# Kernel optimization log

Hardware: AMD Instinct MI355X
Metric: run time of the kernel (lower is better)

Reference implementation:

```python
import jax, jax.numpy as jnp
import numpy as np

N = 50000
E = 800000
IN_CH = 256
ADIM = 64
EDIM = 16
NUM_CLUSTERS = 8


def setup_inputs() -> dict:
    key = jax.random.key(0)
    ks = jax.random.split(key, 16)
    def lin(k, fan_in, fan_out):
        w = jax.random.normal(k, (fan_in, fan_out), jnp.float32) * (fan_in ** -0.5)
        b = jnp.zeros((fan_out,), jnp.float32)
        return w, b
    W_down, b_down = lin(ks[0], IN_CH, ADIM)
    W_up, b_up = lin(ks[1], ADIM, IN_CH)
    W_time, b_time = lin(ks[2], EDIM, ADIM)
    Wq, bq = lin(ks[3], ADIM, ADIM)
    Wk, bk = lin(ks[4], ADIM, ADIM)
    Wv, bv = lin(ks[5], ADIM, ADIM)
    W_out, b_out = lin(ks[6], ADIM, ADIM)
    cluster_emb = jax.random.normal(ks[7], (NUM_CLUSTERS, ADIM), jnp.float32)
    x = jax.random.normal(ks[8], (N, IN_CH), jnp.float32)
    edge_attr = jax.random.normal(ks[9], (E, EDIM), jnp.float32)
    edge_index = jax.random.randint(ks[10], (2, E), 0, N, jnp.int32)
    return {"x": x, "edge_attr": edge_attr, "edge_index": edge_index,
            "W_down": W_down, "b_down": b_down, "W_up": W_up, "b_up": b_up,
            "W_time": W_time, "b_time": b_time, "Wq": Wq, "bq": bq,
            "Wk": Wk, "bk": bk, "Wv": Wv, "bv": bv,
            "cluster_emb": cluster_emb, "W_out": W_out, "b_out": b_out}


def reference(x, edge_attr, edge_index, W_down, b_down, W_up, b_up,
              W_time, b_time, Wq, bq, Wk, bk, Wv, bv, cluster_emb, W_out, b_out):
    n_nodes = x.shape[0]
    scaling = ADIM ** -0.5

    node_feat = jax.nn.relu(x @ W_down + b_down)              # [N, D]
    time_feat = jax.nn.relu(edge_attr @ W_time + b_time)      # [E, D]

    q = node_feat @ Wq + bq                                   # [N, D]
    k = time_feat @ Wk + bk                                   # [E, D]
    v = time_feat @ Wv + bv                                   # [E, D]

    # cluster assignment: argmax of softmax(sim) == argmax of sim
    sims = (time_feat @ cluster_emb.T) * scaling              # [E, C]
    cluster = jnp.argmax(sims, axis=-1).astype(jnp.int32)     # [E]

    src = edge_index[0]                                       # [E]
    q_i = q[src]                                              # [E, D]
    attn = jnp.sum(q_i * k, axis=-1) * scaling                # [E]

    # per-(cluster, src) segments replicate the per-cluster loop exactly
    seg = cluster * n_nodes + src                             # [E]
    num_seg = NUM_CLUSTERS * n_nodes

    # scatter_softmax within each (cluster, src) group (numerically stable)
    m = jax.ops.segment_max(attn, seg, num_segments=num_seg)
    ex = jnp.exp(attn - m[seg])
    denom = jax.ops.segment_sum(ex, seg, num_segments=num_seg)
    w = ex / denom[seg]                                       # [E]

    wv = v * w[:, None]                                       # [E, D]
    sums = jax.ops.segment_sum(wv, seg, num_segments=num_seg)
    sums = sums.reshape(NUM_CLUSTERS, n_nodes, ADIM)
    counts = jax.ops.segment_sum(jnp.ones((E,), jnp.float32), seg, num_segments=num_seg)
    counts = counts.reshape(NUM_CLUSTERS, n_nodes)
    mean = sums / jnp.maximum(counts, 1.0)[..., None]         # scatter_mean (0 where empty)

    # divide by number of non-empty clusters (len(outputs) in torch loop)
    edges_per_cluster = jax.ops.segment_sum(jnp.ones((E,), jnp.float32), cluster,
                                            num_segments=NUM_CLUSTERS)
    n_nonempty = jnp.sum((edges_per_cluster > 0).astype(jnp.float32))
    combined = jnp.sum(mean, axis=0) / n_nonempty             # [N, D]

    fused = jax.nn.relu(combined @ W_out + b_out)             # [N, D]
    out = x + (fused @ W_up + b_up)                           # [N, in_ch]
    return out
```

## Files before the change

### kernel.cpp

```cpp
#include <hip/hip_runtime.h>

#define NN 50000
#define EE 800000
#define INCH 256
#define D 64
#define ED 16
#define NC 8
#define NB 196
#define NEGINF (-3.0e38f)

__device__ __align__(16) char g_ws[64u << 20];

__device__ __forceinline__ unsigned short f2b(float f){
  unsigned u = __float_as_uint(f);
  return (unsigned short)((u + 0x7fffu + ((u >> 16) & 1u)) >> 16);
}
__device__ __forceinline__ unsigned packbf(float lo, float hi){
  return (unsigned)f2b(lo) | ((unsigned)f2b(hi) << 16);
}
__device__ __forceinline__ float blo(unsigned w){ return __uint_as_float(w << 16); }
__device__ __forceinline__ float bhi(unsigned w){ return __uint_as_float(w & 0xffff0000u); }

__global__ __launch_bounds__(256) void Adapter_30872224923942_kernel(
    unsigned* __restrict__ ws, int nwords)
{
  int stride = gridDim.x * 256;
  for (int i = blockIdx.x * 256 + threadIdx.x; i < nwords; i += stride)
    ws[i] = 0u;
}

__global__ __launch_bounds__(256) void kpre(
    const float* __restrict__ Wq, const float* __restrict__ bq,
    const float* __restrict__ Wk, const float* __restrict__ bk,
    const float* __restrict__ Wv, const float* __restrict__ bv,
    const float* __restrict__ Wo, const float* __restrict__ Wd,
    const float* __restrict__ Wu,
    float* __restrict__ M, float* __restrict__ cvec, float* __restrict__ u,
    float* __restrict__ s0, float* __restrict__ Wvo, float* __restrict__ bvo,
    unsigned* __restrict__ WdP, unsigned* __restrict__ WuP)
{
  int b = blockIdx.x, t = threadIdx.x;
  if (b < 16){
    int i = b*4 + (t >> 6), j = t & 63;
    float acc = 0.0f;
    for (int d = 0; d < D; ++d) acc = fmaf(Wq[i*D+d], Wk[j*D+d], acc);
    M[i*D+j] = acc;
  } else if (b < 32){
    int i = (b-16)*4 + (t >> 6), j = t & 63;
    float acc = 0.0f;
    for (int d = 0; d < D; ++d) acc = fmaf(Wv[i*D+d], Wo[d*D+j], acc);
    Wvo[i*D+j] = acc;
  } else if (b < 36){
    for (int k = 0; k < 8; ++k){
      int idx = (b-32)*2048 + t*8 + k;
      int c2 = idx >> 6, j = idx & 63;
      WdP[idx] = packbf(Wd[(2*c2)*D + j], Wd[(2*c2+1)*D + j]);
    }
  } else if (b < 40){
    for (int k = 0; k < 8; ++k){
      int idx = (b-36)*2048 + t*8 + k;
      int d2 = idx >> 8, c = idx & 255;
      WuP[idx] = packbf(Wu[(2*d2)*INCH + c], Wu[(2*d2+1)*INCH + c]);
    }
  } else {
    if (t < 64){
      float acc = 0.0f;
      for (int d = 0; d < D; ++d) acc = fmaf(Wk[t*D+d], bq[d], acc);
      cvec[t] = acc;
    } else if (t < 128){
      int i = t - 64; float acc = 0.0f;
      for (int d = 0; d < D; ++d) acc = fmaf(Wq[i*D+d], bk[d], acc);
      u[i] = acc;
    } else if (t < 192){
      int j = t - 128; float acc = 0.0f;
      for (int d = 0; d < D; ++d) acc = fmaf(bv[d], Wo[d*D+j], acc);
      bvo[j] = acc;
    } else if (t == 192){
      float acc = 0.0f;
      for (int d = 0; d < D; ++d) acc = fmaf(bq[d], bk[d], acc);
      s0[0] = acc;
    }
  }
}

__global__ __launch_bounds__(256) void p1_hist(
    const int* __restrict__ eidx, int* __restrict__ cnt)
{
  int e = blockIdx.x * 256 + threadIdx.x;
  if (e < EE) atomicAdd(&cnt[eidx[e]], 1);
}

__global__ __launch_bounds__(256) void s1_scan(
    const int* __restrict__ cnt, int* __restrict__ rowptr, int* __restrict__ bsum)
{
  __shared__ int s[256];
  int t = threadIdx.x;
  int i = blockIdx.x * 256 + t;
  int v = (i < NN) ? cnt[i] : 0;
  s[t] = v; __syncthreads();
  #pragma unroll
  for (int off = 1; off < 256; off <<= 1){
    int add = (t >= off) ? s[t - off] : 0;
    __syncthreads();
    s[t] += add;
    __syncthreads();
  }
  if (i < NN) rowptr[i] = s[t] - v;
  if (t == 255) bsum[blockIdx.x] = s[255];
}
__global__ __launch_bounds__(256) void s2_scan(int* __restrict__ bsum)
{
  __shared__ int s[256];
  int t = threadIdx.x;
  int v = (t < NB) ? bsum[t] : 0;
  s[t] = v; __syncthreads();
  #pragma unroll
  for (int off = 1; off < 256; off <<= 1){
    int add = (t >= off) ? s[t - off] : 0;
    __syncthreads();
    s[t] += add;
    __syncthreads();
  }
  if (t < NB) bsum[t] = s[t] - v;
}
__global__ __launch_bounds__(256) void s3_add(
    int* __restrict__ rowptr, const int* __restrict__ bsum)
{
  int i = blockIdx.x * 256 + threadIdx.x;
  if (i < NN) rowptr[i] += bsum[blockIdx.x];
  if (i == 0) rowptr[NN] = EE;
}

__global__ __launch_bounds__(256) void p2_build(
    const int* __restrict__ eidx, const int* __restrict__ rowptr,
    int* __restrict__ fill, int2* __restrict__ pairS)
{
  int e = blockIdx.x * 256 + threadIdx.x;
  if (e >= EE) return;
  int src = eidx[e];
  int r = atomicAdd(&fill[src], 1);
  int2 pr; pr.x = e; pr.y = src;
  pairS[rowptr[src] + r] = pr;
}

__global__ __launch_bounds__(256) void k1_node(
    const float* __restrict__ x, const unsigned* __restrict__ WdP,
    const float* __restrict__ bd, const float* __restrict__ M,
    const float* __restrict__ cvec, const float* __restrict__ u,
    const float* __restrict__ s0p,
    unsigned short* __restrict__ qkH, float* __restrict__ qb)
{
  __shared__ unsigned sWdP[8192];
  __shared__ float sX[16][256];
  __shared__ float sNf[16][64];
  int t = threadIdx.x;
  int lane = t & 63;
  int wg = __builtin_amdgcn_readfirstlane(t >> 6);
  int n0 = blockIdx.x * 16 + wg * 4;
  #pragma unroll
  for (int r = 0; r < 4; ++r){
    const float* gsrc = x + (size_t)(n0 + r) * INCH + lane * 4;
    __builtin_amdgcn_global_load_lds(
        (const __attribute__((address_space(1))) void*)gsrc,
        (__attribute__((address_space(3))) void*)&sX[wg*4 + r][0],
        16, 0, 0);
  }
  #pragma unroll
  for (int i = 0; i < 8; ++i)
    ((uint4*)sWdP)[t + 256*i] = ((const uint4*)WdP)[t + 256*i];
  __syncthreads();
  const float4* xr0 = (const float4*)&sX[wg*4 + 0][0];
  const float4* xr1 = (const float4*)&sX[wg*4 + 1][0];
  const float4* xr2 = (const float4*)&sX[wg*4 + 2][0];
  const float4* xr3 = (const float4*)&sX[wg*4 + 3][0];
  float bdl = bd[lane];
  float a0 = bdl, a1 = bdl, a2 = bdl, a3 = bdl;
  #pragma unroll 4
  for (int c4 = 0; c4 < 64; ++c4){
    float4 x0 = xr0[c4], x1 = xr1[c4], x2 = xr2[c4], x3 = xr3[c4];
    unsigned wA = sWdP[(c4*2  )*64 + lane];
    unsigned wB = sWdP[(c4*2+1)*64 + lane];
    float w0 = blo(wA), w1 = bhi(wA), w2 = blo(wB), w3 = bhi(wB);
    a0 = fmaf(x0.x,w0,a0); a0 = fmaf(x0.y,w1,a0); a0 = fmaf(x0.z,w2,a0); a0 = fmaf(x0.w,w3,a0);
    a1 = fmaf(x1.x,w0,a1); a1 = fmaf(x1.y,w1,a1); a1 = fmaf(x1.z,w2,a1); a1 = fmaf(x1.w,w3,a1);
    a2 = fmaf(x2.x,w0,a2); a2 = fmaf(x2.y,w1,a2); a2 = fmaf(x2.z,w2,a2); a2 = fmaf(x2.w,w3,a2);
    a3 = fmaf(x3.x,w0,a3); a3 = fmaf(x3.y,w1,a3); a3 = fmaf(x3.z,w2,a3); a3 = fmaf(x3.w,w3,a3);
  }
  float n0f = fmaxf(a0, 0.0f), n1f = fmaxf(a1, 0.0f);
  float n2f = fmaxf(a2, 0.0f), n3f = fmaxf(a3, 0.0f);
  sNf[wg*4+0][lane] = n0f;
  sNf[wg*4+1][lane] = n1f;
  sNf[wg*4+2][lane] = n2f;
  sNf[wg*4+3][lane] = n3f;
  float cvl = cvec[lane];
  float q0 = cvl, q1 = cvl, q2 = cvl, q3 = cvl;
  const float4* f0 = (const float4*)&sNf[wg*4+0][0];
  const float4* f1 = (const float4*)&sNf[wg*4+1][0];
  const float4* f2 = (const float4*)&sNf[wg*4+2][0];
  const float4* f3 = (const float4*)&sNf[wg*4+3][0];
  #pragma unroll 4
  for (int i4 = 0; i4 < 16; ++i4){
    float4 v0 = f0[i4], v1 = f1[i4], v2 = f2[i4], v3 = f3[i4];
    float m0 = M[(4*i4+0)*64 + lane];
    float m1 = M[(4*i4+1)*64 + lane];
    float m2 = M[(4*i4+2)*64 + lane];
    float m3 = M[(4*i4+3)*64 + lane];
    q0 = fmaf(v0.x,m0,q0); q0 = fmaf(v0.y,m1,q0); q0 = fmaf(v0.z,m2,q0); q0 = fmaf(v0.w,m3,q0);
    q1 = fmaf(v1.x,m0,q1); q1 = fmaf(v1.y,m1,q1); q1 = fmaf(v1.z,m2,q1); q1 = fmaf(v1.w,m3,q1);
    q2 = fmaf(v2.x,m0,q2); q2 = fmaf(v2.y,m1,q2); q2 = fmaf(v2.z,m2,q2); q2 = fmaf(v2.w,m3,q2);
    q3 = fmaf(v3.x,m0,q3); q3 = fmaf(v3.y,m1,q3); q3 = fmaf(v3.z,m2,q3); q3 = fmaf(v3.w,m3,q3);
  }
  qkH[(size_t)(n0+0)*D + lane] = f2b(q0);
  qkH[(size_t)(n0+1)*D + lane] = f2b(q1);
  qkH[(size_t)(n0+2)*D + lane] = f2b(q2);
  qkH[(size_t)(n0+3)*D + lane] = f2b(q3);
  float ul = u[lane], s00 = s0p[0];
  float b0 = n0f*ul, b1 = n1f*ul, b2 = n2f*ul, b3 = n3f*ul;
  #pragma unroll
  for (int s = 32; s; s >>= 1){
    b0 += __shfl_xor(b0, s); b1 += __shfl_xor(b1, s);
    b2 += __shfl_xor(b2, s); b3 += __shfl_xor(b3, s);
  }
  if (lane == 0){
    qb[n0+0] = b0 + s00; qb[n0+1] = b1 + s00;
    qb[n0+2] = b2 + s00; qb[n0+3] = b3 + s00;
  }
}

__global__ __launch_bounds__(256) void p3_edge(
    const float* __restrict__ ea, const int* __restrict__ eidx,
    const float* __restrict__ Wt, const float* __restrict__ bt, const float* __restrict__ ce,
    const unsigned short* __restrict__ qkH, const float* __restrict__ qb,
    float* __restrict__ attnE, unsigned char* __restrict__ clE,
    unsigned* __restrict__ epc)
{
  __shared__ unsigned s_epc[NC];
  int t = threadIdx.x;
  if (t < NC) s_epc[t] = 0u;
  __syncthreads();
  int e0 = blockIdx.x * 512 + t;
  int e1 = e0 + 256;
  bool v1 = (e1 < EE);
  int e1c = v1 ? e1 : e0;
  int sA = eidx[e0];
  int sB = eidx[e1c];
  const float4* pa = (const float4*)(ea + (size_t)e0 * ED);
  float4 A0 = pa[0], A1 = pa[1], A2 = pa[2], A3 = pa[3];
  float qb0 = qb[sA];
  const float4* pb = (const float4*)(ea + (size_t)e1c * ED);
  float4 B0 = pb[0], B1 = pb[1], B2 = pb[2], B3 = pb[3];
  float qb1 = qb[sB];
  uint4 QA[8], QB[8];
  {
    const uint4* qp = (const uint4*)(qkH + (size_t)sA * D);
    #pragma unroll
    for (int i = 0; i < 8; ++i) QA[i] = qp[i];
  }
  {
    const uint4* qp = (const uint4*)(qkH + (size_t)sB * D);
    #pragma unroll
    for (int i = 0; i < 8; ++i) QB[i] = qp[i];
  }
  const float4* Wt4 = (const float4*)Wt;
  const float4* bt4 = (const float4*)bt;
  const float4* ce4 = (const float4*)ce;

  {
    float eav[ED] = {A0.x,A0.y,A0.z,A0.w, A1.x,A1.y,A1.z,A1.w,
                     A2.x,A2.y,A2.z,A2.w, A3.x,A3.y,A3.z,A3.w};
    float sims[NC];
    #pragma unroll
    for (int c = 0; c < NC; ++c) sims[c] = 0.0f;
    float at = qb0;
    #pragma unroll
    for (int d4 = 0; d4 < D/4; ++d4){
      float4 acc = bt4[d4];
      #pragma unroll
      for (int j = 0; j < ED; ++j){
        float4 wv = Wt4[j*(D/4) + d4];
        acc.x = fmaf(eav[j], wv.x, acc.x);
        acc.y = fmaf(eav[j], wv.y, acc.y);
        acc.z = fmaf(eav[j], wv.z, acc.z);
        acc.w = fmaf(eav[j], wv.w, acc.w);
      }
      float t0 = fmaxf(acc.x, 0.0f), t1 = fmaxf(acc.y, 0.0f);
      float t2 = fmaxf(acc.z, 0.0f), t3 = fmaxf(acc.w, 0.0f);
      #pragma unroll
      for (int c = 0; c < NC; ++c){
        float4 cv = ce4[c*(D/4) + d4];
        sims[c] = fmaf(t0, cv.x, sims[c]);
        sims[c] = fmaf(t1, cv.y, sims[c]);
        sims[c] = fmaf(t2, cv.z, sims[c]);
        sims[c] = fmaf(t3, cv.w, sims[c]);
      }
      uint4 qv = QA[d4 >> 1];
      unsigned w0 = (d4 & 1) ? qv.z : qv.x;
      unsigned w1 = (d4 & 1) ? qv.w : qv.y;
      at = fmaf(blo(w0), t0, at);
      at = fmaf(bhi(w0), t1, at);
      at = fmaf(blo(w1), t2, at);
      at = fmaf(bhi(w1), t3, at);
    }
    float best = NEGINF; int bc = 0;
    #pragma unroll
    for (int c = 0; c < NC; ++c){
      if (sims[c] > best){ best = sims[c]; bc = c; }
    }
    at *= 0.125f;
    attnE[e0] = at;
    clE[e0] = (unsigned char)bc;
    atomicAdd(&s_epc[bc], 1u);
  }

  if (v1){
    float eav[ED] = {B0.x,B0.y,B0.z,B0.w, B1.x,B1.y,B1.z,B1.w,
                     B2.x,B2.y,B2.z,B2.w, B3.x,B3.y,B3.z,B3.w};
    float sims[NC];
    #pragma unroll
    for (int c = 0; c < NC; ++c) sims[c] = 0.0f;
    float at = qb1;
    #pragma unroll
    for (int d4 = 0; d4 < D/4; ++d4){
      float4 acc = bt4[d4];
      #pragma unroll
      for (int j = 0; j < ED; ++j){
        float4 wv = Wt4[j*(D/4) + d4];
        acc.x = fmaf(eav[j], wv.x, acc.x);
        acc.y = fmaf(eav[j], wv.y, acc.y);
        acc.z = fmaf(eav[j], wv.z, acc.z);
        acc.w = fmaf(eav[j], wv.w, acc.w);
      }
      float t0 = fmaxf(acc.x, 0.0f), t1 = fmaxf(acc.y, 0.0f);
      float t2 = fmaxf(acc.z, 0.0f), t3 = fmaxf(acc.w, 0.0f);
      #pragma unroll
      for (int c = 0; c < NC; ++c){
        float4 cv = ce4[c*(D/4) + d4];
        sims[c] = fmaf(t0, cv.x, sims[c]);
        sims[c] = fmaf(t1, cv.y, sims[c]);
        sims[c] = fmaf(t2, cv.z, sims[c]);
        sims[c] = fmaf(t3, cv.w, sims[c]);
      }
      uint4 qv = QB[d4 >> 1];
      unsigned w0 = (d4 & 1) ? qv.z : qv.x;
      unsigned w1 = (d4 & 1) ? qv.w : qv.y;
      at = fmaf(blo(w0), t0, at);
      at = fmaf(bhi(w0), t1, at);
      at = fmaf(blo(w1), t2, at);
      at = fmaf(bhi(w1), t3, at);
    }
    float best = NEGINF; int bc = 0;
    #pragma unroll
    for (int c = 0; c < NC; ++c){
      if (sims[c] > best){ best = sims[c]; bc = c; }
    }
    at *= 0.125f;
    attnE[e1] = at;
    clE[e1] = (unsigned char)bc;
    atomicAdd(&s_epc[bc], 1u);
  }

  __syncthreads();
  if (t < NC){
    unsigned v = s_epc[t];
    if (v) atomicAdd(&epc[t], v);
  }
}

#define EROW 20
__global__ __launch_bounds__(256) void p4_node(
    const float* __restrict__ ea, const int2* __restrict__ pairS,
    const float* __restrict__ Wt, const float* __restrict__ bt,
    const float* __restrict__ attnE, const unsigned char* __restrict__ clE,
    const int* __restrict__ rowptr,
    float* __restrict__ T, float* __restrict__ S)
{
  __shared__ float s_den[4][NC];
  __shared__ int   s_cnt[4][NC];
  __shared__ float s_inv[4][NC];
  __shared__ float s_coef[4][64];
  __shared__ float s_ea[4][64][EROW];
  int t = threadIdx.x, lane = t & 63, w = t >> 6;
  float wl[ED];
  #pragma unroll
  for (int j = 0; j < ED; ++j) wl[j] = Wt[j*D + lane];
  float btl = bt[lane];
  if (lane < NC){ s_den[w][lane] = 0.0f; s_cnt[w][lane] = 0; }
  int node = blockIdx.x * 4 + w;
  int start = rowptr[node], end = rowptr[node + 1];
  for (int base = start; base < end; base += 64){
    int idx = base + lane;
    if (idx < end){
      int e = pairS[idx].x;
      float ex = __expf(attnE[e]);
      int c = clE[e];
      atomicAdd(&s_den[w][c], ex);
      atomicAdd(&s_cnt[w][c], 1);
    }
  }
  if (lane < NC){
    int   cc = s_cnt[w][lane];
    float dd = s_den[w][lane];
    s_inv[w][lane] = (cc > 0) ? 1.0f / (dd * (float)cc) : 0.0f;
    float sv = (cc > 0) ? 1.0f / (float)cc : 0.0f;
    sv += __shfl_xor(sv, 1); sv += __shfl_xor(sv, 2); sv += __shfl_xor(sv, 4);
    if (lane == 0) S[node] = sv;
  }
  float Tacc = 0.0f;
  for (int base = start; base < end; base += 64){
    int idx = base + lane;
    if (idx < end){
      int e = pairS[idx].x;
      s_coef[w][lane] = __expf(attnE[e]) * s_inv[w][clE[e]];
    }
    #pragma unroll
    for (int r = 0; r < 4; ++r){
      int slot = base + r*16 + (lane >> 2);
      if (slot < end){
        int e = pairS[slot].x;
        float4 v = ((const float4*)ea)[(size_t)e*4 + (lane & 3)];
        *(float4*)&s_ea[w][slot - base][(lane & 3)*4] = v;
      }
    }
    int mm = min(64, end - base);
    for (int tt = 0; tt < mm; ++tt){
      float coef = s_coef[w][tt];
      const float4* er = (const float4*)&s_ea[w][tt][0];
      float4 e0 = er[0], e1 = er[1], e2 = er[2], e3 = er[3];
      float tfv = btl;
      tfv = fmaf(e0.x, wl[0], tfv);  tfv = fmaf(e0.y, wl[1], tfv);
      tfv = fmaf(e0.z, wl[2], tfv);  tfv = fmaf(e0.w, wl[3], tfv);
      tfv = fmaf(e1.x, wl[4], tfv);  tfv = fmaf(e1.y, wl[5], tfv);
      tfv = fmaf(e1.z, wl[6], tfv);  tfv = fmaf(e1.w, wl[7], tfv);
      tfv = fmaf(e2.x, wl[8], tfv);  tfv = fmaf(e2.y, wl[9], tfv);
      tfv = fmaf(e2.z, wl[10], tfv); tfv = fmaf(e2.w, wl[11], tfv);
      tfv = fmaf(e3.x, wl[12], tfv); tfv = fmaf(e3.y, wl[13], tfv);
      tfv = fmaf(e3.z, wl[14], tfv); tfv = fmaf(e3.w, wl[15], tfv);
      tfv = fmaxf(tfv, 0.0f);
      Tacc = fmaf(coef, tfv, Tacc);
    }
  }
  T[(size_t)node * D + lane] = Tacc;
}

__global__ __launch_bounds__(256) void k5_out(
    const float* __restrict__ x, const float* __restrict__ T, const float* __restrict__ S,
    const float* __restrict__ Wvo, const float* __restrict__ bvo,
    const unsigned* __restrict__ WuP, const float* __restrict__ bu,
    const float* __restrict__ bo, const unsigned* __restrict__ epc,
    float* __restrict__ out)
{
  __shared__ unsigned sWuP[8192];
  __shared__ float s_fu[16*64];
  int t = threadIdx.x;
  #pragma unroll
  for (int i = 0; i < 8; ++i)
    ((uint4*)sWuP)[t + 256*i] = ((const uint4*)WuP)[t + 256*i];
  int lane = t & 63;
  int wg = __builtin_amdgcn_readfirstlane(t >> 6);
  int n0 = blockIdx.x * 16 + wg * 4;
  float nne = 0.0f;
  #pragma unroll
  for (int c = 0; c < NC; ++c) nne += (epc[c] > 0u) ? 1.0f : 0.0f;
  float inv = 1.0f / fmaxf(nne, 1.0f);
  float T0 = T[(size_t)(n0+0)*D + lane];
  float T1 = T[(size_t)(n0+1)*D + lane];
  float T2 = T[(size_t)(n0+2)*D + lane];
  float T3 = T[(size_t)(n0+3)*D + lane];
  float bvl = bvo[lane], bol = bo[lane];
  float f0 = S[n0+0]*bvl, f1 = S[n0+1]*bvl, f2 = S[n0+2]*bvl, f3 = S[n0+3]*bvl;
  #pragma unroll 8
  for (int i = 0; i < 64; ++i){
    float wv = Wvo[i*64 + lane];
    f0 = fmaf(__shfl(T0, i), wv, f0);
    f1 = fmaf(__shfl(T1, i), wv, f1);
    f2 = fmaf(__shfl(T2, i), wv, f2);
    f3 = fmaf(__shfl(T3, i), wv, f3);
  }
  f0 = fmaxf(f0*inv + bol, 0.0f);
  f1 = fmaxf(f1*inv + bol, 0.0f);
  f2 = fmaxf(f2*inv + bol, 0.0f);
  f3 = fmaxf(f3*inv + bol, 0.0f);
  s_fu[(wg*4+0)*64 + lane] = f0;
  s_fu[(wg*4+1)*64 + lane] = f1;
  s_fu[(wg*4+2)*64 + lane] = f2;
  s_fu[(wg*4+3)*64 + lane] = f3;
  __syncthreads();
  float4 bu4 = ((const float4*)bu)[lane];
  float4 o0 = ((const float4*)(x + (size_t)(n0+0)*INCH))[lane];
  float4 o1 = ((const float4*)(x + (size_t)(n0+1)*INCH))[lane];
  float4 o2 = ((const float4*)(x + (size_t)(n0+2)*INCH))[lane];
  float4 o3 = ((const float4*)(x + (size_t)(n0+3)*INCH))[lane];
  o0.x += bu4.x; o0.y += bu4.y; o0.z += bu4.z; o0.w += bu4.w;
  o1.x += bu4.x; o1.y += bu4.y; o1.z += bu4.z; o1.w += bu4.w;
  o2.x += bu4.x; o2.y += bu4.y; o2.z += bu4.z; o2.w += bu4.w;
  o3.x += bu4.x; o3.y += bu4.y; o3.z += bu4.z; o3.w += bu4.w;
  const float2* fu2 = (const float2*)s_fu;
  #pragma unroll 4
  for (int d2 = 0; d2 < 32; ++d2){
    uint4 wp = *(const uint4*)&sWuP[d2*256 + lane*4];
    float4 wlv = { blo(wp.x), blo(wp.y), blo(wp.z), blo(wp.w) };
    float4 wh  = { bhi(wp.x), bhi(wp.y), bhi(wp.z), bhi(wp.w) };
    float2 g0 = fu2[(wg*4+0)*32 + d2];
    float2 g1 = fu2[(wg*4+1)*32 + d2];
    float2 g2 = fu2[(wg*4+2)*32 + d2];
    float2 g3 = fu2[(wg*4+3)*32 + d2];
    o0.x = fmaf(g0.x, wlv.x, o0.x); o0.y = fmaf(g0.x, wlv.y, o0.y);
    o0.z = fmaf(g0.x, wlv.z, o0.z); o0.w = fmaf(g0.x, wlv.w, o0.w);
    o0.x = fmaf(g0.y, wh.x, o0.x);  o0.y = fmaf(g0.y, wh.y, o0.y);
    o0.z = fmaf(g0.y, wh.z, o0.z);  o0.w = fmaf(g0.y, wh.w, o0.w);
    o1.x = fmaf(g1.x, wlv.x, o1.x); o1.y = fmaf(g1.x, wlv.y, o1.y);
    o1.z = fmaf(g1.x, wlv.z, o1.z); o1.w = fmaf(g1.x, wlv.w, o1.w);
    o1.x = fmaf(g1.y, wh.x, o1.x);  o1.y = fmaf(g1.y, wh.y, o1.y);
    o1.z = fmaf(g1.y, wh.z, o1.z);  o1.w = fmaf(g1.y, wh.w, o1.w);
    o2.x = fmaf(g2.x, wlv.x, o2.x); o2.y = fmaf(g2.x, wlv.y, o2.y);
    o2.z = fmaf(g2.x, wlv.z, o2.z); o2.w = fmaf(g2.x, wlv.w, o2.w);
    o2.x = fmaf(g2.y, wh.x, o2.x);  o2.y = fmaf(g2.y, wh.y, o2.y);
    o2.z = fmaf(g2.y, wh.z, o2.z);  o2.w = fmaf(g2.y, wh.w, o2.w);
    o3.x = fmaf(g3.x, wlv.x, o3.x); o3.y = fmaf(g3.x, wlv.y, o3.y);
    o3.z = fmaf(g3.x, wlv.z, o3.z); o3.w = fmaf(g3.x, wlv.w, o3.w);
    o3.x = fmaf(g3.y, wh.x, o3.x);  o3.y = fmaf(g3.y, wh.y, o3.y);
    o3.z = fmaf(g3.y, wh.z, o3.z);  o3.w = fmaf(g3.y, wh.w, o3.w);
  }
  ((float4*)(out + (size_t)(n0+0)*INCH))[lane] = o0;
  ((float4*)(out + (size_t)(n0+1)*INCH))[lane] = o1;
  ((float4*)(out + (size_t)(n0+2)*INCH))[lane] = o2;
  ((float4*)(out + (size_t)(n0+3)*INCH))[lane] = o3;
}

extern "C" void kernel_launch(void* const* d_in, const int* in_sizes, int n_in,
                              void* d_out, int out_size, void* d_ws, size_t ws_size,
                              hipStream_t stream)
{
  const float* x  = (const float*)d_in[0];
  const float* ea = (const float*)d_in[1];
  const int* eidx = (const int*)d_in[2];
  const float* Wd = (const float*)d_in[3];  const float* bd = (const float*)d_in[4];
  const float* Wu = (const float*)d_in[5];  const float* bu = (const float*)d_in[6];
  const float* Wt = (const float*)d_in[7];  const float* bt = (const float*)d_in[8];
  const float* Wq = (const float*)d_in[9];  const float* bq = (const float*)d_in[10];
  const float* Wk = (const float*)d_in[11]; const float* bk = (const float*)d_in[12];
  const float* Wv = (const float*)d_in[13]; const float* bv = (const float*)d_in[14];
  const float* ce = (const float*)d_in[15];
  const float* Wo = (const float*)d_in[16]; const float* bo = (const float*)d_in[17];
  float* out = (float*)d_out;

  size_t need = 0;
  need += (size_t)NN*4;
  need += (size_t)NN*4;
  need += 64;
  size_t zbytes = need;
  need += (size_t)(NN+4)*4;
  need += 1024;
  need += (size_t)NN*D*2;
  need += (size_t)NN*4;
  need += (size_t)EE*8;
  need += (size_t)EE*4;
  need += (size_t)EE;
  need += (size_t)NN*D*4;
  need += (size_t)NN*4;
  need += 4096*4 + 256 + 256 + 16 + 4096*4 + 256;
  need += 8192*4 + 8192*4;

  char* w = (char*)d_ws;
  if (ws_size < need){
    void* p = nullptr;
    hipGetSymbolAddress(&p, HIP_SYMBOL(g_ws));
    w = (char*)p;
  }
  size_t off = 0;
  int*      cnt    = (int*)(w + off);      off += (size_t)NN*4;
  int*      fill   = (int*)(w + off);      off += (size_t)NN*4;
  unsigned* epc    = (unsigned*)(w + off); off += 64;
  int*      rowptr = (int*)(w + off);      off += (size_t)(NN+4)*4;
  int*      bsum   = (int*)(w + off);      off += 1024;
  unsigned short* qkH = (unsigned short*)(w + off); off += (size_t)NN*D*2;
  float*    qb     = (float*)(w + off);    off += (size_t)NN*4;
  int2*     pairS  = (int2*)(w + off);     off += (size_t)EE*8;
  float*    attnE  = (float*)(w + off);    off += (size_t)EE*4;
  unsigned char* clE = (unsigned char*)(w + off); off += (size_t)EE;
  off = (off + 15) & ~(size_t)15;
  float*    T      = (float*)(w + off);    off += (size_t)NN*D*4;
  float*    S      = (float*)(w + off);    off += (size_t)NN*4;
  float*    M      = (float*)(w + off);    off += 4096*4;
  float*    cvec   = (float*)(w + off);    off += 256;
  float*    u      = (float*)(w + off);    off += 256;
  float*    s0     = (float*)(w + off);    off += 16;
  float*    Wvo    = (float*)(w + off);    off += 4096*4;
  float*    bvo    = (float*)(w + off);    off += 256;
  unsigned* WdP    = (unsigned*)(w + off); off += 8192*4;
  unsigned* WuP    = (unsigned*)(w + off); off += 8192*4;

  int zwords = (int)(zbytes / 4);
  Adapter_30872224923942_kernel<<<dim3(128), dim3(256), 0, stream>>>((unsigned*)w, zwords);
  kpre<<<dim3(41), dim3(256), 0, stream>>>(Wq, bq, Wk, bk, Wv, bv, Wo, Wd, Wu,
                                           M, cvec, u, s0, Wvo, bvo, WdP, WuP);
  p1_hist<<<dim3(EE/256), dim3(256), 0, stream>>>(eidx, cnt);
  s1_scan<<<dim3(NB), dim3(256), 0, stream>>>(cnt, rowptr, bsum);
  s2_scan<<<dim3(1),  dim3(256), 0, stream>>>(bsum);
  s3_add <<<dim3(NB), dim3(256), 0, stream>>>(rowptr, bsum);
  p2_build<<<dim3(EE/256), dim3(256), 0, stream>>>(eidx, rowptr, fill, pairS);
  k1_node<<<dim3(NN/16), dim3(256), 0, stream>>>(x, WdP, bd, M, cvec, u, s0, qkH, qb);
  p3_edge<<<dim3((EE + 511)/512), dim3(256), 0, stream>>>(ea, eidx, Wt, bt, ce, qkH, qb,
                                                          attnE, clE, epc);
  p4_node<<<dim3(NN/4), dim3(256), 0, stream>>>(ea, pairS, Wt, bt, attnE, clE, rowptr, T, S);
  k5_out <<<dim3(NN/16), dim3(256), 0, stream>>>(x, T, S, Wvo, bvo, WuP, bu, bo, epc, out);
}
```

Baseline: 446.2 us.

## Move node projection GEMMs in k1_node onto bf16 MFMA with split precision

Rewrites k1_node so the x@W_down and node_feat@M products run on 16x16x32 bf16 MFMA instructions, with hi/lo bf16 splitting of the activations (and of M) to approximate fp32 accuracy. Weights are pre-transposed and packed in kpre and stored in LDS with an XOR swizzle to avoid bank conflicts. Each block now processes 64 rows instead of 16, which amortizes the weight staging. The aim is to replace scalar FMA work with matrix-core throughput, at the cost of extra MFMAs for the split terms and more register pressure from loading x directly into registers.

```diff
diff --git a/kernel.cpp b/kernel.cpp
--- a/kernel.cpp
+++ b/kernel.cpp
@@ -11,6 +11,9 @@
 
 __device__ __align__(16) char g_ws[64u << 20];
 
+typedef __attribute__((ext_vector_type(8))) short bf16x8;
+typedef __attribute__((ext_vector_type(4))) float f32x4;
+
 __device__ __forceinline__ unsigned short f2b(float f){
   unsigned u = __float_as_uint(f);
   return (unsigned short)((u + 0x7fffu + ((u >> 16) & 1u)) >> 16);
@@ -20,6 +23,27 @@
 }
 __device__ __forceinline__ float blo(unsigned w){ return __uint_as_float(w << 16); }
 __device__ __forceinline__ float bhi(unsigned w){ return __uint_as_float(w & 0xffff0000u); }
+
+union FragU { unsigned u[4]; uint4 q; bf16x8 b; };
+__device__ __forceinline__ bf16x8 as_frag(unsigned a, unsigned b, unsigned c, unsigned d){
+  FragU t; t.u[0]=a; t.u[1]=b; t.u[2]=c; t.u[3]=d; return t.b;
+}
+__device__ __forceinline__ bf16x8 ld_frag(const unsigned* p){
+  FragU t; t.q = *(const uint4*)p; return t.b;
+}
+__device__ __forceinline__ void split2(float a, float b, unsigned &hi, unsigned &lo){
+  hi = packbf(a, b);
+  lo = packbf(a - blo(hi), b - bhi(hi));
+}
+__device__ __forceinline__ void mk_frags(float4 e0, float4 e1, bf16x8 &Ah, bf16x8 &Al){
+  unsigned h0,h1,h2,h3,l0,l1,l2,l3;
+  split2(e0.x, e0.y, h0, l0);
+  split2(e0.z, e0.w, h1, l1);
+  split2(e1.x, e1.y, h2, l2);
+  split2(e1.z, e1.w, h3, l3);
+  Ah = as_frag(h0,h1,h2,h3);
+  Al = as_frag(l0,l1,l2,l3);
+}
 
 __global__ __launch_bounds__(256) void Adapter_30872224923942_kernel(
     unsigned* __restrict__ ws, int nwords)
@@ -35,32 +59,39 @@
     const float* __restrict__ Wv, const float* __restrict__ bv,
     const float* __restrict__ Wo, const float* __restrict__ Wd,
     const float* __restrict__ Wu,
-    float* __restrict__ M, float* __restrict__ cvec, float* __restrict__ u,
+    float* __restrict__ cvec, float* __restrict__ u,
     float* __restrict__ s0, float* __restrict__ Wvo, float* __restrict__ bvo,
-    unsigned* __restrict__ WdP, unsigned* __restrict__ WuP)
+    unsigned* __restrict__ WdTP, unsigned* __restrict__ WuP,
+    unsigned* __restrict__ MThP, unsigned* __restrict__ MTlP)
 {
   int b = blockIdx.x, t = threadIdx.x;
   if (b < 16){
     int i = b*4 + (t >> 6), j = t & 63;
     float acc = 0.0f;
-    for (int d = 0; d < D; ++d) acc = fmaf(Wq[i*D+d], Wk[j*D+d], acc);
-    M[i*D+j] = acc;
-  } else if (b < 32){
-    int i = (b-16)*4 + (t >> 6), j = t & 63;
-    float acc = 0.0f;
     for (int d = 0; d < D; ++d) acc = fmaf(Wv[i*D+d], Wo[d*D+j], acc);
     Wvo[i*D+j] = acc;
-  } else if (b < 36){
+  } else if (b < 20){
     for (int k = 0; k < 8; ++k){
-      int idx = (b-32)*2048 + t*8 + k;
-      int c2 = idx >> 6, j = idx & 63;
-      WdP[idx] = packbf(Wd[(2*c2)*D + j], Wd[(2*c2+1)*D + j]);
-    }
-  } else if (b < 40){
+      int idx = (b-16)*2048 + t*8 + k;
+      int col = idx >> 7, kw = idx & 127;
+      WdTP[idx] = packbf(Wd[(2*kw)*D + col], Wd[(2*kw+1)*D + col]);
+    }
+  } else if (b < 24){
     for (int k = 0; k < 8; ++k){
-      int idx = (b-36)*2048 + t*8 + k;
+      int idx = (b-20)*2048 + t*8 + k;
       int d2 = idx >> 8, c = idx & 255;
       WuP[idx] = packbf(Wu[(2*d2)*INCH + c], Wu[(2*d2+1)*INCH + c]);
+    }
+  } else if (b < 26){
+    for (int k = 0; k < 4; ++k){
+      int idx = (b-24)*1024 + t*4 + k;
+      int j = idx >> 5, kw = idx & 31;
+      float m0 = 0.0f, m1 = 0.0f;
+      for (int d = 0; d < D; ++d) m0 = fmaf(Wq[(2*kw  )*D+d], Wk[j*D+d], m0);
+      for (int d = 0; d < D; ++d) m1 = fmaf(Wq[(2*kw+1)*D+d], Wk[j*D+d], m1);
+      unsigned hi = packbf(m0, m1);
+      MThP[idx] = hi;
+      MTlP[idx] = packbf(m0 - blo(hi), m1 - bhi(hi));
     }
   } else {
     if (t < 64){
@@ -144,86 +175,117 @@
 }
 
 __global__ __launch_bounds__(256) void k1_node(
-    const float* __restrict__ x, const unsigned* __restrict__ WdP,
-    const float* __restrict__ bd, const float* __restrict__ M,
+    const float* __restrict__ x, const unsigned* __restrict__ WdTP,
+    const float* __restrict__ bd,
+    const unsigned* __restrict__ MThP, const unsigned* __restrict__ MTlP,
     const float* __restrict__ cvec, const float* __restrict__ u,
     const float* __restrict__ s0p,
     unsigned short* __restrict__ qkH, float* __restrict__ qb)
 {
-  __shared__ unsigned sWdP[8192];
-  __shared__ float sX[16][256];
-  __shared__ float sNf[16][64];
+  __shared__ unsigned sWdT[8192];
+  __shared__ unsigned sMTh[2048];
+  __shared__ unsigned sMTl[2048];
+  __shared__ float sNf[4][16][68];
   int t = threadIdx.x;
   int lane = t & 63;
-  int wg = __builtin_amdgcn_readfirstlane(t >> 6);
-  int n0 = blockIdx.x * 16 + wg * 4;
-  #pragma unroll
-  for (int r = 0; r < 4; ++r){
-    const float* gsrc = x + (size_t)(n0 + r) * INCH + lane * 4;
-    __builtin_amdgcn_global_load_lds(
-        (const __attribute__((address_space(1))) void*)gsrc,
-        (__attribute__((address_space(3))) void*)&sX[wg*4 + r][0],
-        16, 0, 0);
-  }
-  #pragma unroll
-  for (int i = 0; i < 8; ++i)
-    ((uint4*)sWdP)[t + 256*i] = ((const uint4*)WdP)[t + 256*i];
+  int w = t >> 6;
+  int colA = lane & 15;
+  int g = lane >> 4;
+  int row0 = blockIdx.x * 64 + w * 16;
+
+  int arow = row0 + colA;
+  const float* xp = x + (size_t)min(arow, NN-1) * INCH + (g << 3);
+  float4 xv[16];
+  #pragma unroll
+  for (int s = 0; s < 8; ++s){
+    xv[2*s  ] = ((const float4*)(xp + s*32))[0];
+    xv[2*s+1] = ((const float4*)(xp + s*32))[1];
+  }
+  #pragma unroll
+  for (int i = 0; i < 8; ++i){
+    int idx = 4*(t + 256*i);
+    int col = idx >> 7;
+    int dst = (idx & ~127) | ((idx & 127) ^ ((col & 7) << 2));
+    *(uint4*)&sWdT[dst] = ((const uint4*)WdTP)[t + 256*i];
+  }
+  #pragma unroll
+  for (int i = 0; i < 2; ++i){
+    int idx = 4*(t + 256*i);
+    int col = idx >> 5;
+    int dst = (idx & ~31) | ((idx & 31) ^ ((col & 7) << 2));
+    *(uint4*)&sMTh[dst] = ((const uint4*)MThP)[t + 256*i];
+    *(uint4*)&sMTl[dst] = ((const uint4*)MTlP)[t + 256*i];
+  }
   __syncthreads();
-  const float4* xr0 = (const float4*)&sX[wg*4 + 0][0];
-  const float4* xr1 = (const float4*)&sX[wg*4 + 1][0];
-  const float4* xr2 = (const float4*)&sX[wg*4 + 2][0];
-  const float4* xr3 = (const float4*)&sX[wg*4 + 3][0];
-  float bdl = bd[lane];
-  float a0 = bdl, a1 = bdl, a2 = bdl, a3 = bdl;
-  #pragma unroll 4
-  for (int c4 = 0; c4 < 64; ++c4){
-    float4 x0 = xr0[c4], x1 = xr1[c4], x2 = xr2[c4], x3 = xr3[c4];
-    unsigned wA = sWdP[(c4*2  )*64 + lane];
-    unsigned wB = sWdP[(c4*2+1)*64 + lane];
-    float w0 = blo(wA), w1 = bhi(wA), w2 = blo(wB), w3 = bhi(wB);
-    a0 = fmaf(x0.x,w0,a0); a0 = fmaf(x0.y,w1,a0); a0 = fmaf(x0.z,w2,a0); a0 = fmaf(x0.w,w3,a0);
-    a1 = fmaf(x1.x,w0,a1); a1 = fmaf(x1.y,w1,a1); a1 = fmaf(x1.z,w2,a1); a1 = fmaf(x1.w,w3,a1);
-    a2 = fmaf(x2.x,w0,a2); a2 = fmaf(x2.y,w1,a2); a2 = fmaf(x2.z,w2,a2); a2 = fmaf(x2.w,w3,a2);
-    a3 = fmaf(x3.x,w0,a3); a3 = fmaf(x3.y,w1,a3); a3 = fmaf(x3.z,w2,a3); a3 = fmaf(x3.w,w3,a3);
-  }
-  float n0f = fmaxf(a0, 0.0f), n1f = fmaxf(a1, 0.0f);
-  float n2f = fmaxf(a2, 0.0f), n3f = fmaxf(a3, 0.0f);
-  sNf[wg*4+0][lane] = n0f;
-  sNf[wg*4+1][lane] = n1f;
-  sNf[wg*4+2][lane] = n2f;
-  sNf[wg*4+3][lane] = n3f;
-  float cvl = cvec[lane];
-  float q0 = cvl, q1 = cvl, q2 = cvl, q3 = cvl;
-  const float4* f0 = (const float4*)&sNf[wg*4+0][0];
-  const float4* f1 = (const float4*)&sNf[wg*4+1][0];
-  const float4* f2 = (const float4*)&sNf[wg*4+2][0];
-  const float4* f3 = (const float4*)&sNf[wg*4+3][0];
-  #pragma unroll 4
-  for (int i4 = 0; i4 < 16; ++i4){
-    float4 v0 = f0[i4], v1 = f1[i4], v2 = f2[i4], v3 = f3[i4];
-    float m0 = M[(4*i4+0)*64 + lane];
-    float m1 = M[(4*i4+1)*64 + lane];
-    float m2 = M[(4*i4+2)*64 + lane];
-    float m3 = M[(4*i4+3)*64 + lane];
-    q0 = fmaf(v0.x,m0,q0); q0 = fmaf(v0.y,m1,q0); q0 = fmaf(v0.z,m2,q0); q0 = fmaf(v0.w,m3,q0);
-    q1 = fmaf(v1.x,m0,q1); q1 = fmaf(v1.y,m1,q1); q1 = fmaf(v1.z,m2,q1); q1 = fmaf(v1.w,m3,q1);
-    q2 = fmaf(v2.x,m0,q2); q2 = fmaf(v2.y,m1,q2); q2 = fmaf(v2.z,m2,q2); q2 = fmaf(v2.w,m3,q2);
-    q3 = fmaf(v3.x,m0,q3); q3 = fmaf(v3.y,m1,q3); q3 = fmaf(v3.z,m2,q3); q3 = fmaf(v3.w,m3,q3);
-  }
-  qkH[(size_t)(n0+0)*D + lane] = f2b(q0);
-  qkH[(size_t)(n0+1)*D + lane] = f2b(q1);
-  qkH[(size_t)(n0+2)*D + lane] = f2b(q2);
-  qkH[(size_t)(n0+3)*D + lane] = f2b(q3);
-  float ul = u[lane], s00 = s0p[0];
-  float b0 = n0f*ul, b1 = n1f*ul, b2 = n2f*ul, b3 = n3f*ul;
-  #pragma unroll
-  for (int s = 32; s; s >>= 1){
-    b0 += __shfl_xor(b0, s); b1 += __shfl_xor(b1, s);
-    b2 += __shfl_xor(b2, s); b3 += __shfl_xor(b3, s);
-  }
-  if (lane == 0){
-    qb[n0+0] = b0 + s00; qb[n0+1] = b1 + s00;
-    qb[n0+2] = b2 + s00; qb[n0+3] = b3 + s00;
+
+  f32x4 acc[4];
+  #pragma unroll
+  for (int nt = 0; nt < 4; ++nt){
+    float bdc = bd[nt*16 + colA];
+    acc[nt] = (f32x4){bdc, bdc, bdc, bdc};
+  }
+  #pragma unroll
+  for (int s = 0; s < 8; ++s){
+    bf16x8 Ah, Al;
+    mk_frags(xv[2*s], xv[2*s+1], Ah, Al);
+    #pragma unroll
+    for (int nt = 0; nt < 4; ++nt){
+      int col = nt*16 + colA;
+      int kw = s*16 + g*4;
+      bf16x8 B = ld_frag(&sWdT[col*128 + (kw ^ ((col & 7) << 2))]);
+      acc[nt] = __builtin_amdgcn_mfma_f32_16x16x32_bf16(Ah, B, acc[nt], 0, 0, 0);
+      acc[nt] = __builtin_amdgcn_mfma_f32_16x16x32_bf16(Al, B, acc[nt], 0, 0, 0);
+    }
+  }
+  #pragma unroll
+  for (int nt = 0; nt < 4; ++nt){
+    #pragma unroll
+    for (int q = 0; q < 4; ++q)
+      sNf[w][g*4 + q][nt*16 + colA] = fmaxf(acc[nt][q], 0.0f);
+  }
+
+  {
+    const float* nr = &sNf[w][colA][g*16];
+    float b = 0.0f;
+    #pragma unroll
+    for (int c = 0; c < 16; ++c) b = fmaf(nr[c], u[g*16 + c], b);
+    b += __shfl_xor(b, 16);
+    b += __shfl_xor(b, 32);
+    int qrow = row0 + colA;
+    if (lane < 16 && qrow < NN) qb[qrow] = b + s0p[0];
+  }
+
+  f32x4 acc2[4];
+  #pragma unroll
+  for (int nt = 0; nt < 4; ++nt){
+    float cvl = cvec[nt*16 + colA];
+    acc2[nt] = (f32x4){cvl, cvl, cvl, cvl};
+  }
+  #pragma unroll
+  for (int s = 0; s < 2; ++s){
+    const float* ar = &sNf[w][colA][s*32 + g*8];
+    float4 e0 = *(const float4*)(ar);
+    float4 e1 = *(const float4*)(ar + 4);
+    bf16x8 Ah, Al;
+    mk_frags(e0, e1, Ah, Al);
+    #pragma unroll
+    for (int nt = 0; nt < 4; ++nt){
+      int col = nt*16 + colA;
+      int kw = s*16 + g*4;
+      bf16x8 Bh = ld_frag(&sMTh[col*32 + (kw ^ ((col & 7) << 2))]);
+      bf16x8 Bl = ld_frag(&sMTl[col*32 + (kw ^ ((col & 7) << 2))]);
+      acc2[nt] = __builtin_amdgcn_mfma_f32_16x16x32_bf16(Ah, Bh, acc2[nt], 0, 0, 0);
+      acc2[nt] = __builtin_amdgcn_mfma_f32_16x16x32_bf16(Al, Bh, acc2[nt], 0, 0, 0);
+      acc2[nt] = __builtin_amdgcn_mfma_f32_16x16x32_bf16(Ah, Bl, acc2[nt], 0, 0, 0);
+    }
+  }
+  #pragma unroll
+  for (int nt = 0; nt < 4; ++nt){
+    #pragma unroll
+    for (int q = 0; q < 4; ++q){
+      int r = row0 + g*4 + q;
+      if (r < NN) qkH[(size_t)r * D + nt*16 + colA] = f2b(acc2[nt][q]);
+    }
   }
 }
 
@@ -556,10 +618,12 @@
   need += (size_t)EE*8;
   need += (size_t)EE*4;
   need += (size_t)EE;
+  need += 16;
   need += (size_t)NN*D*4;
   need += (size_t)NN*4;
-  need += 4096*4 + 256 + 256 + 16 + 4096*4 + 256;
+  need += 256 + 256 + 16 + 4096*4 + 256;
   need += 8192*4 + 8192*4;
+  need += 2048*4 + 2048*4;
 
   char* w = (char*)d_ws;
   if (ws_size < need){
@@ -581,25 +645,27 @@
   off = (off + 15) & ~(size_t)15;
   float*    T      = (float*)(w + off);    off += (size_t)NN*D*4;
   float*    S      = (float*)(w + off);    off += (size_t)NN*4;
-  float*    M      = (float*)(w + off);    off += 4096*4;
   float*    cvec   = (float*)(w + off);    off += 256;
   float*    u      = (float*)(w + off);    off += 256;
   float*    s0     = (float*)(w + off);    off += 16;
   float*    Wvo    = (float*)(w + off);    off += 4096*4;
   float*    bvo    = (float*)(w + off);    off += 256;
-  unsigned* WdP    = (unsigned*)(w + off); off += 8192*4;
+  unsigned* WdTP   = (unsigned*)(w + off); off += 8192*4;
   unsigned* WuP    = (unsigned*)(w + off); off += 8192*4;
+  unsigned* MThP   = (unsigned*)(w + off); off += 2048*4;
+  unsigned* MTlP   = (unsigned*)(w + off); off += 2048*4;
 
   int zwords = (int)(zbytes / 4);
   Adapter_30872224923942_kernel<<<dim3(128), dim3(256), 0, stream>>>((unsigned*)w, zwords);
-  kpre<<<dim3(41), dim3(256), 0, stream>>>(Wq, bq, Wk, bk, Wv, bv, Wo, Wd, Wu,
-                                           M, cvec, u, s0, Wvo, bvo, WdP, WuP);
+  kpre<<<dim3(27), dim3(256), 0, stream>>>(Wq, bq, Wk, bk, Wv, bv, Wo, Wd, Wu,
+                                           cvec, u, s0, Wvo, bvo, WdTP, WuP, MThP, MTlP);
   p1_hist<<<dim3(EE/256), dim3(256), 0, stream>>>(eidx, cnt);
   s1_scan<<<dim3(NB), dim3(256), 0, stream>>>(cnt, rowptr, bsum);
   s2_scan<<<dim3(1),  dim3(256), 0, stream>>>(bsum);
   s3_add <<<dim3(NB), dim3(256), 0, stream>>>(rowptr, bsum);
   p2_build<<<dim3(EE/256), dim3(256), 0, stream>>>(eidx, rowptr, fill, pairS);
-  k1_node<<<dim3(NN/16), dim3(256), 0, stream>>>(x, WdP, bd, M, cvec, u, s0, qkH, qb);
+  k1_node<<<dim3((NN + 63)/64), dim3(256), 0, stream>>>(x, WdTP, bd, MThP, MTlP,
+                                                        cvec, u, s0, qkH, qb);
   p3_edge<<<dim3((EE + 511)/512), dim3(256), 0, stream>>>(ea, eidx, Wt, bt, ce, qkH, qb,
                                                           attnE, clE, epc);
   p4_node<<<dim3(NN/4), dim3(256), 0, stream>>>(ea, pairS, Wt, bt, attnE, clE, rowptr, T, S);
```

New measurement: 432.1 us. -3.2%, faster.
